# Performance work log

Hardware: AMD Instinct MI355X
Metric: run time of the kernel (lower is better)

The kernel has to match this reference:

```python
import jax, jax.numpy as jnp
import numpy as np

NUM_HEADS = 12
HEAD_DIM = 64
DROPKEY = 0.1
BN_EPS = 1e-5


def setup_inputs() -> dict:
    key = jax.random.key(0)
    ks = jax.random.split(key, 6)
    b, n, d = 4, 1024, 768
    img_c, hw = 256, 32
    x = jax.random.normal(ks[0], (b, n, d), dtype=jnp.float32)
    y = jax.random.normal(ks[1], (b, img_c, hw, hw), dtype=jnp.float32)
    drop_mask = jax.random.uniform(ks[2], (b, NUM_HEADS, n, n), dtype=jnp.float32)
    W_qkv = jax.random.normal(ks[3], (d, 3 * d), dtype=jnp.float32) * (d ** -0.5)
    conv1_w = jax.random.normal(ks[4], (img_c, 1, 3, 3), dtype=jnp.float32) * 0.1
    conv2_w = jax.random.normal(ks[5], (d, img_c, 1, 1), dtype=jnp.float32) * (img_c ** -0.5)
    bn_gamma = jnp.ones((d,), dtype=jnp.float32)
    bn_beta = jnp.zeros((d,), dtype=jnp.float32)
    return {"x": x, "y": y, "drop_mask": drop_mask, "W_qkv": W_qkv,
            "conv1_w": conv1_w, "conv2_w": conv2_w,
            "bn_gamma": bn_gamma, "bn_beta": bn_beta}


def reference(x, y, drop_mask, W_qkv, conv1_w, conv2_w, bn_gamma, bn_beta):
    b, n, d = x.shape
    h, hd = NUM_HEADS, HEAD_DIM
    scale = hd ** -0.5

    # --- attention branch ---
    qkv = x @ W_qkv                                     # [b, n, 3d]
    q, k, v = jnp.split(qkv, 3, axis=-1)
    def to_heads(t):
        return t.reshape(b, n, h, hd).transpose(0, 2, 1, 3)  # [b, h, n, hd]
    q, k, v = to_heads(q), to_heads(k), to_heads(v)
    scores = jnp.einsum('bhid,bhjd->bhij', q, k) * scale
    # dropkey: bernoulli(p) additive -1e12 mask before softmax
    mask = (drop_mask < DROPKEY).astype(scores.dtype)
    scores = scores + mask * jnp.asarray(-1e12, scores.dtype)
    attn = jax.nn.softmax(scores, axis=-1)
    out = jnp.einsum('bhij,bhjd->bhid', attn, v)        # [b, h, n, hd]
    out = out.transpose(0, 2, 1, 3).reshape(b, n, h * hd)

    # --- conv branch: depthwise 3x3 -> 1x1 -> BN(train) -> ReLU ---
    img_c = y.shape[1]
    y1 = jax.lax.conv_general_dilated(
        y, conv1_w, window_strides=(1, 1), padding='SAME',
        dimension_numbers=('NCHW', 'OIHW', 'NCHW'),
        feature_group_count=img_c)                      # [b, img_c, H, W]
    y2 = jax.lax.conv_general_dilated(
        y1, conv2_w, window_strides=(1, 1), padding='SAME',
        dimension_numbers=('NCHW', 'OIHW', 'NCHW'))     # [b, d, H, W]
    mean = jnp.mean(y2, axis=(0, 2, 3), keepdims=True)
    var = jnp.var(y2, axis=(0, 2, 3), keepdims=True)
    y_bn = (y2 - mean) * jax.lax.rsqrt(var + BN_EPS)
    y_bn = y_bn * bn_gamma[None, :, None, None] + bn_beta[None, :, None, None]
    y_out = jax.nn.relu(y_bn)                           # [b, d, H, W]

    # patchify(p1=p2=1) + flatten == 'b c h w -> b (h w) c'
    y_tok = y_out.transpose(0, 2, 3, 1).reshape(b, n, d)
    return (out + y_tok, y_out)


if __name__ == '__main__':
    inp = setup_inputs()
    o, yo = jax.jit(reference)(**inp)
    print(o.shape, yo.shape)
```

## Files before the change

kernel.cpp:

```cpp
#include <hip/hip_runtime.h>
#include <cstddef>

#define B_     4
#define NTOK   1024
#define DMODEL 768
#define NH     12
#define IMGC   256
#define NPIX   1024

typedef __attribute__((ext_vector_type(8))) short bf16x8;
typedef __attribute__((ext_vector_type(4))) float f32x4;
typedef __attribute__((ext_vector_type(8))) unsigned short u16x8;

static __device__ __forceinline__ unsigned short f2bf(float f) {
  unsigned int u = __float_as_uint(f);
  u += 0x7FFFu + ((u >> 16) & 1u);
  return (unsigned short)(u >> 16);
}

#define SWZ(row, b) (((row) << 7) + ((b) ^ (((row) & 7) << 4)))

#define GLOAD16(g, l) __builtin_amdgcn_global_load_lds(                      \
    (const __attribute__((address_space(1))) void*)(g),                      \
    (__attribute__((address_space(3))) void*)(l), 16, 0, 0)

__global__ __launch_bounds__(256) void k_cvt(const float* __restrict__ X,
                                             const float* __restrict__ Wqkv,
                                             const float* __restrict__ W2,
                                             unsigned short* __restrict__ Xb,
                                             unsigned short* __restrict__ Wtb,
                                             unsigned short* __restrict__ W2b,
                                             float* __restrict__ bnacc) {
  __shared__ unsigned short T[32][33];
  const int bid = blockIdx.x;
  const int t = threadIdx.x;
  if (bid < 1536) {
    const size_t i8 = (size_t)bid * 256 + t;
    const float4 a = *(const float4*)(X + i8 * 8);
    const float4 b = *(const float4*)(X + i8 * 8 + 4);
    u16x8 o;
    o[0] = f2bf(a.x); o[1] = f2bf(a.y); o[2] = f2bf(a.z); o[3] = f2bf(a.w);
    o[4] = f2bf(b.x); o[5] = f2bf(b.y); o[6] = f2bf(b.z); o[7] = f2bf(b.w);
    *(u16x8*)(Xb + i8 * 8) = o;
  } else if (bid < 3264) {
    const int b2 = bid - 1536;
    const int n0 = (b2 % 72) * 32, k0 = (b2 / 72) * 32;
    const int tx = t & 31, ty = t >> 5;
#pragma unroll
    for (int i = 0; i < 4; i++) {
      int kl = ty + i * 8;
      T[tx][kl] = f2bf(Wqkv[(size_t)(k0 + kl) * 2304 + n0 + tx]);
    }
    __syncthreads();
#pragma unroll
    for (int i = 0; i < 4; i++) {
      int nl = ty + i * 8;
      Wtb[(size_t)(n0 + nl) * 768 + k0 + tx] = T[nl][tx];
    }
  } else if (bid < 3360) {
    const size_t i8 = (size_t)(bid - 3264) * 256 + t;
    const float4 a = *(const float4*)(W2 + i8 * 8);
    const float4 b = *(const float4*)(W2 + i8 * 8 + 4);
    u16x8 o;
    o[0] = f2bf(a.x); o[1] = f2bf(a.y); o[2] = f2bf(a.z); o[3] = f2bf(a.w);
    o[4] = f2bf(b.x); o[5] = f2bf(b.y); o[6] = f2bf(b.z); o[7] = f2bf(b.w);
    *(u16x8*)(W2b + i8 * 8) = o;
  } else {
    for (int i = t; i < 1536; i += 256) bnacc[i] = 0.0f;
  }
}

__global__ __launch_bounds__(256) void k_qkv_gemm(const unsigned short* __restrict__ Xb,
                                                  const unsigned short* __restrict__ Wt,
                                                  unsigned short* __restrict__ q,
                                                  unsigned short* __restrict__ k,
                                                  unsigned short* __restrict__ v) {
  __shared__ __align__(16) char AsB[16384];
  __shared__ __align__(16) char BsB[16384];
  const int t = threadIdx.x;
  const int w = t >> 6, l = t & 63;
  const int r = l & 15, g = l >> 4;
  const int wr = w >> 1, wc = w & 1;
  const int m0 = blockIdx.y * 128;
  const int n0 = blockIdx.x * 128;
  const int rsel  = l >> 3;
  const int slotp = (l & 7) ^ (rsel & 7);
  f32x4 acc[4][4] = {};

  for (int step = 0; step < 12; ++step) {
    const int k0 = step * 64;
#pragma unroll
    for (int i = 0; i < 4; i++) {
      const int chunk = (i << 2) + w;
      const int row = (chunk << 3) + rsel;
      GLOAD16(Xb + (size_t)(m0 + row) * 768 + k0 + (slotp << 3),
              AsB + (chunk << 10) + (l << 4));
      GLOAD16(Wt + (size_t)(n0 + row) * 768 + k0 + (slotp << 3),
              BsB + (chunk << 10) + (l << 4));
    }
    __syncthreads();
#pragma unroll
    for (int kk = 0; kk < 2; kk++) {
      bf16x8 a[4], b[4];
#pragma unroll
      for (int m = 0; m < 4; m++) {
        const int row = wr * 64 + m * 16 + r;
        a[m] = *(const bf16x8*)(AsB + SWZ(row, kk * 64 + (g << 4)));
      }
#pragma unroll
      for (int n = 0; n < 4; n++) {
        const int row = wc * 64 + n * 16 + r;
        b[n] = *(const bf16x8*)(BsB + SWZ(row, kk * 64 + (g << 4)));
      }
#pragma unroll
      for (int m = 0; m < 4; m++)
#pragma unroll
        for (int n = 0; n < 4; n++)
          acc[m][n] = __builtin_amdgcn_mfma_f32_16x16x32_bf16(a[m], b[n], acc[m][n], 0, 0, 0);
    }
    __syncthreads();
  }

  const int which = blockIdx.x / 6;
  const int cbase = (blockIdx.x - which * 6) * 128 + wc * 64;
  unsigned short* dst = which == 0 ? q : (which == 1 ? k : v);
#pragma unroll
  for (int m = 0; m < 4; m++) {
    const int grow = m0 + wr * 64 + m * 16 + g * 4;
#pragma unroll
    for (int n = 0; n < 4; n++) {
      const int c = cbase + n * 16 + r;
      const int head = c >> 6, dim = c & 63;
#pragma unroll
      for (int reg = 0; reg < 4; reg++) {
        const int row = grow + reg;
        const int bb = row >> 10, tok = row & 1023;
        dst[((size_t)(((bb * NH + head) << 10) + tok) << 6) + dim] = f2bf(acc[m][n][reg]);
      }
    }
  }
}

__global__ __launch_bounds__(256) void k_attn(const unsigned short* __restrict__ qb,
                                              const unsigned short* __restrict__ kb,
                                              const unsigned short* __restrict__ vb,
                                              const float* __restrict__ dm,
                                              float* __restrict__ out0) {
  __shared__ __align__(16) unsigned short QsA[4096];
  __shared__ __align__(16) unsigned short KsA[4096];
  __shared__ __align__(16) unsigned short VtA[4096];
  __shared__ __align__(16) unsigned short PsA[4096];
  char* qs = (char*)QsA; char* ks = (char*)KsA;
  char* vt = (char*)VtA; char* ps = (char*)PsA;
  const int bh = blockIdx.x;
  const int qt = blockIdx.y;
  const int t  = threadIdx.x;
  const int w = t >> 6, l = t & 63, r = l & 15, g = l >> 4;
  const size_t hbase = (size_t)bh << 16;
  const char* qg = (const char*)(qb + hbase + ((size_t)qt << 12));
  const char* kg = (const char*)(kb + hbase);
  const char* vg = (const char*)(vb + hbase);
  const float* mp = dm + ((size_t)bh << 20) + ((size_t)(qt * 64) << 10);

#pragma unroll
  for (int i = 0; i < 2; i++) {
    int cid = t + (i << 8);
    int row = cid >> 3, slot = cid & 7;
    uint4 val = *(const uint4*)(qg + row * 128 + slot * 16);
    *(uint4*)(qs + SWZ(row, slot * 16)) = val;
  }

  float m_run[4] = {-INFINITY, -INFINITY, -INFINITY, -INFINITY};
  float l_run[4] = {0.0f, 0.0f, 0.0f, 0.0f};
  f32x4 O[4] = {};

  for (int kt = 0; kt < 16; kt++) {
    __syncthreads();
#pragma unroll
    for (int i = 0; i < 2; i++) {
      int cid = t + (i << 8);
      int row = cid >> 3, slot = cid & 7;
      uint4 val = *(const uint4*)(kg + (size_t)(kt * 64 + row) * 128 + slot * 16);
      *(uint4*)(ks + SWZ(row, slot * 16)) = val;
    }
    {
      int j = t & 63, dh = t >> 6;
      const char* vrow = vg + (size_t)(kt * 64 + j) * 128 + dh * 32;
      u16x8 v0 = *(const u16x8*)(vrow);
      u16x8 v1 = *(const u16x8*)(vrow + 16);
#pragma unroll
      for (int e = 0; e < 8; e++) {
        *(unsigned short*)(vt + SWZ(dh * 16 + e, 2 * j))     = v0[e];
        *(unsigned short*)(vt + SWZ(dh * 16 + 8 + e, 2 * j)) = v1[e];
      }
    }
    float md[4][4];
    {
      const float* mr = mp + (size_t)(w * 16 + g * 4) * 1024 + kt * 64 + r;
#pragma unroll
      for (int reg = 0; reg < 4; reg++)
#pragma unroll
        for (int jt = 0; jt < 4; jt++)
          md[reg][jt] = mr[reg * 1024 + jt * 16];
    }
    __syncthreads();

    f32x4 s[4] = {};
    bf16x8 aQ[2];
#pragma unroll
    for (int kc = 0; kc < 2; kc++)
      aQ[kc] = *(const bf16x8*)(qs + SWZ(w * 16 + r, kc * 64 + g * 16));
#pragma unroll
    for (int jt = 0; jt < 4; jt++) {
#pragma unroll
      for (int kc = 0; kc < 2; kc++) {
        bf16x8 bK = *(const bf16x8*)(ks + SWZ(jt * 16 + r, kc * 64 + g * 16));
        s[jt] = __builtin_amdgcn_mfma_f32_16x16x32_bf16(aQ[kc], bK, s[jt], 0, 0, 0);
      }
    }
    float sv[4][4];
#pragma unroll
    for (int jt = 0; jt < 4; jt++)
#pragma unroll
      for (int reg = 0; reg < 4; reg++)
        sv[jt][reg] = s[jt][reg] * 0.125f + (md[reg][jt] < 0.1f ? -1e12f : 0.0f);

    float alpha[4];
#pragma unroll
    for (int reg = 0; reg < 4; reg++) {
      float mt = fmaxf(fmaxf(sv[0][reg], sv[1][reg]), fmaxf(sv[2][reg], sv[3][reg]));
      mt = fmaxf(mt, __shfl_xor(mt, 1));
      mt = fmaxf(mt, __shfl_xor(mt, 2));
      mt = fmaxf(mt, __shfl_xor(mt, 4));
      mt = fmaxf(mt, __shfl_xor(mt, 8));
      float mn = fmaxf(m_run[reg], mt);
      alpha[reg] = __expf(m_run[reg] - mn);
      m_run[reg] = mn;
    }
#pragma unroll
    for (int reg = 0; reg < 4; reg++) {
      int row = w * 16 + g * 4 + reg;
      float ps_ = 0.0f;
#pragma unroll
      for (int jt = 0; jt < 4; jt++) {
        float p = __expf(sv[jt][reg] - m_run[reg]);
        ps_ += p;
        *(unsigned short*)(ps + SWZ(row, 2 * (jt * 16 + r))) = f2bf(p);
      }
      ps_ += __shfl_xor(ps_, 1);
      ps_ += __shfl_xor(ps_, 2);
      ps_ += __shfl_xor(ps_, 4);
      ps_ += __shfl_xor(ps_, 8);
      l_run[reg] = l_run[reg] * alpha[reg] + ps_;
    }
#pragma unroll
    for (int dt = 0; dt < 4; dt++)
#pragma unroll
      for (int reg = 0; reg < 4; reg++)
        O[dt][reg] *= alpha[reg];
    asm volatile("s_waitcnt lgkmcnt(0)" ::: "memory");
    __builtin_amdgcn_sched_barrier(0);
#pragma unroll
    for (int kc = 0; kc < 2; kc++) {
      bf16x8 aP = *(const bf16x8*)(ps + SWZ(w * 16 + r, kc * 64 + g * 16));
#pragma unroll
      for (int dt = 0; dt < 4; dt++) {
        bf16x8 bV = *(const bf16x8*)(vt + SWZ(dt * 16 + r, kc * 64 + g * 16));
        O[dt] = __builtin_amdgcn_mfma_f32_16x16x32_bf16(aP, bV, O[dt], 0, 0, 0);
      }
    }
  }
  const int bb = bh / NH, hh = bh % NH;
  float inv[4];
#pragma unroll
  for (int reg = 0; reg < 4; reg++) inv[reg] = 1.0f / l_run[reg];
  float* op = out0 + ((size_t)(bb * 1024 + qt * 64 + w * 16 + g * 4)) * 768 + hh * 64 + r;
#pragma unroll
  for (int reg = 0; reg < 4; reg++)
#pragma unroll
    for (int dt = 0; dt < 4; dt++)
      op[(size_t)reg * 768 + dt * 16] = O[dt][reg] * inv[reg];
}

__global__ __launch_bounds__(256) void k_dwconv(const float* __restrict__ y,
                                                const float* __restrict__ w1,
                                                float* __restrict__ y1) {
  const int bc = blockIdx.x;
  const int c = bc & 255;
  const float* yin = y + (size_t)bc * NPIX;
  float* yout = y1 + (size_t)bc * NPIX;
  float w[9];
#pragma unroll
  for (int i = 0; i < 9; i++) w[i] = w1[c * 9 + i];
  const int t = threadIdx.x;
#pragma unroll
  for (int rep = 0; rep < 4; rep++) {
    int px = t + rep * 256;
    int yy = px >> 5, xx = px & 31;
    float acc = 0.0f;
#pragma unroll
    for (int dy = -1; dy <= 1; dy++) {
      int sy = yy + dy;
      if (sy < 0 || sy > 31) continue;
#pragma unroll
      for (int dx = -1; dx <= 1; dx++) {
        int sx = xx + dx;
        if (sx < 0 || sx > 31) continue;
        acc = fmaf(yin[(sy << 5) + sx], w[(dy + 1) * 3 + dx + 1], acc);
      }
    }
    yout[px] = acc;
  }
}

__global__ __launch_bounds__(256) void k_trans(const float* __restrict__ y1,
                                               unsigned short* __restrict__ y1t) {
  __shared__ float T[64][65];
  const int p0 = blockIdx.x * 64, c0 = blockIdx.y * 64, b = blockIdx.z;
  const int t = threadIdx.x;
  const float* src = y1 + ((size_t)b << 18);
  {
    const int pl = t & 63, cl0 = t >> 6;
#pragma unroll
    for (int i = 0; i < 16; i++) {
      int cl = cl0 * 16 + i;
      T[cl][pl] = src[(size_t)(c0 + cl) * 1024 + p0 + pl];
    }
  }
  __syncthreads();
  {
    const int cl = t & 63, pl0 = t >> 6;
    unsigned short* dst = y1t + ((size_t)b << 18);
#pragma unroll
    for (int i = 0; i < 16; i++) {
      int pl = pl0 * 16 + i;
      dst[(size_t)(p0 + pl) * 256 + c0 + cl] = f2bf(T[cl][pl]);
    }
  }
}

__global__ __launch_bounds__(256) void k_c1x1(const unsigned short* __restrict__ W2b,
                                              const unsigned short* __restrict__ y1t,
                                              float* __restrict__ Y2,
                                              float* __restrict__ bn_sum,
                                              float* __restrict__ bn_sumsq) {
  __shared__ __align__(16) char AsB[16384];
  __shared__ __align__(16) char BsB[16384];
  const int t = threadIdx.x;
  const int w = t >> 6, l = t & 63;
  const int r = l & 15, g = l >> 4;
  const int wr = w >> 1, wc = w & 1;
  const int m0 = blockIdx.y * 128;
  const int n0 = blockIdx.x * 128;
  const int b  = blockIdx.z;
  const unsigned short* Bb = y1t + ((size_t)b << 18);
  const int rsel  = l >> 3;
  const int slotp = (l & 7) ^ (rsel & 7);
  f32x4 acc[4][4] = {};

  for (int step = 0; step < 4; ++step) {
    const int k0 = step * 64;
#pragma unroll
    for (int i = 0; i < 4; i++) {
      const int chunk = (i << 2) + w;
      const int row = (chunk << 3) + rsel;
      GLOAD16(W2b + (size_t)(m0 + row) * 256 + k0 + (slotp << 3),
              AsB + (chunk << 10) + (l << 4));
      GLOAD16(Bb + (size_t)(n0 + row) * 256 + k0 + (slotp << 3),
              BsB + (chunk << 10) + (l << 4));
    }
    __syncthreads();
#pragma unroll
    for (int kk = 0; kk < 2; kk++) {
      bf16x8 a[4], bfr[4];
#pragma unroll
      for (int m = 0; m < 4; m++) {
        const int row = wr * 64 + m * 16 + r;
        a[m] = *(const bf16x8*)(AsB + SWZ(row, kk * 64 + (g << 4)));
      }
#pragma unroll
      for (int n = 0; n < 4; n++) {
        const int row = wc * 64 + n * 16 + r;
        bfr[n] = *(const bf16x8*)(BsB + SWZ(row, kk * 64 + (g << 4)));
      }
#pragma unroll
      for (int m = 0; m < 4; m++)
#pragma unroll
        for (int n = 0; n < 4; n++)
          acc[m][n] = __builtin_amdgcn_mfma_f32_16x16x32_bf16(a[m], bfr[n], acc[m][n], 0, 0, 0);
    }
    __syncthreads();
  }

  float* Yb = Y2 + (((size_t)b * DMODEL) << 10);
#pragma unroll
  for (int m = 0; m < 4; m++) {
#pragma unroll
    for (int reg = 0; reg < 4; reg++) {
      const int oc = m0 + wr * 64 + m * 16 + g * 4 + reg;
      float s = 0.0f, sq = 0.0f;
#pragma unroll
      for (int n = 0; n < 4; n++) {
        const int p = n0 + wc * 64 + n * 16 + r;
        const float val = acc[m][n][reg];
        Yb[((size_t)oc << 10) + p] = val;
        s += val;
        sq = fmaf(val, val, sq);
      }
      s  += __shfl_xor(s, 1);  sq += __shfl_xor(sq, 1);
      s  += __shfl_xor(s, 2);  sq += __shfl_xor(sq, 2);
      s  += __shfl_xor(s, 4);  sq += __shfl_xor(sq, 4);
      s  += __shfl_xor(s, 8);  sq += __shfl_xor(sq, 8);
      if (r == 0) {
        atomicAdd(&bn_sum[oc], s);
        atomicAdd(&bn_sumsq[oc], sq);
      }
    }
  }
}

__global__ __launch_bounds__(256) void k_bnfuse(const float* __restrict__ y2,
                                                const float* __restrict__ bn_sum,
                                                const float* __restrict__ bn_sumsq,
                                                const float* __restrict__ gamma,
                                                const float* __restrict__ beta,
                                                float* __restrict__ out0,
                                                float* __restrict__ out1) {
  __shared__ float T[32][33];
  __shared__ float sc_l[32], sh_l[32];
  const int p0 = blockIdx.x * 32;
  const int c0 = blockIdx.y * 32;
  const int bb = blockIdx.z;
  const int tx = threadIdx.x;
  const int ty = threadIdx.y;
  const int tt = ty * 32 + tx;
  if (tt < 32) {
    const int c = c0 + tt;
    float S = bn_sum[c], SQ = bn_sumsq[c];
    float mean = S * (1.0f / 4096.0f);
    float var = SQ * (1.0f / 4096.0f) - mean * mean;
    float rstd = rsqrtf(var + 1e-5f);
    float s = gamma[c] * rstd;
    sc_l[tt] = s;
    sh_l[tt] = fmaf(-mean, s, beta[c]);
  }
  __syncthreads();
#pragma unroll
  for (int i = 0; i < 4; i++) {
    int cl = ty + 8 * i;
    int c = c0 + cl;
    size_t a = ((size_t)(bb * DMODEL + c) << 10) + p0 + tx;
    float val = fmaxf(fmaf(y2[a], sc_l[cl], sh_l[cl]), 0.0f);
    out1[a] = val;
    T[cl][tx] = val;
  }
  __syncthreads();
#pragma unroll
  for (int i = 0; i < 4; i++) {
    int pl = ty + 8 * i;
    size_t a = ((size_t)((bb << 10) + p0 + pl)) * DMODEL + c0 + tx;
    out0[a] += T[tx][pl];
  }
}

extern "C" void kernel_launch(void* const* d_in, const int* in_sizes, int n_in,
                              void* d_out, int out_size, void* d_ws, size_t ws_size,
                              hipStream_t stream) {
  (void)in_sizes; (void)n_in; (void)out_size; (void)ws_size;
  const float* x    = (const float*)d_in[0];
  const float* y    = (const float*)d_in[1];
  const float* dm   = (const float*)d_in[2];
  const float* wqkv = (const float*)d_in[3];
  const float* w1   = (const float*)d_in[4];
  const float* w2   = (const float*)d_in[5];
  const float* gam  = (const float*)d_in[6];
  const float* bet  = (const float*)d_in[7];
  float* out0 = (float*)d_out;
  float* out1 = out0 + (size_t)B_ * NTOK * DMODEL;

  char* wsb = (char*)d_ws;
  unsigned short* Xb  = (unsigned short*)wsb;
  unsigned short* Wtb = (unsigned short*)(wsb + 6291456);
  unsigned short* W2b = (unsigned short*)(wsb + 9830400);
  unsigned short* qb  = (unsigned short*)(wsb + 10223616);
  unsigned short* kb  = (unsigned short*)(wsb + 16515072);
  unsigned short* vb  = (unsigned short*)(wsb + 22806528);
  unsigned short* y1t = (unsigned short*)(wsb + 29097984);
  float* y2 = (float*)(wsb + 31195136);
  float* y1 = (float*)(wsb + 35389440);
  float* bnacc = (float*)(wsb + 43778048);
  float* bn_sum = bnacc;
  float* bn_sumsq = bnacc + 768;

  k_cvt<<<dim3(3361), 256, 0, stream>>>(x, wqkv, w2, Xb, Wtb, W2b, bnacc);
  k_dwconv<<<dim3(B_ * IMGC), 256, 0, stream>>>(y, w1, y1);
  k_trans<<<dim3(16, 4, B_), 256, 0, stream>>>(y1, y1t);
  k_c1x1<<<dim3(8, 6, B_), 256, 0, stream>>>(W2b, y1t, y2, bn_sum, bn_sumsq);
  k_qkv_gemm<<<dim3(18, 32), 256, 0, stream>>>(Xb, Wtb, qb, kb, vb);
  k_attn<<<dim3(48, 16), 256, 0, stream>>>(qb, kb, vb, dm, out0);
  k_bnfuse<<<dim3(32, 24, B_), dim3(32, 8), 0, stream>>>(y2, bn_sum, bn_sumsq, gam, bet, out0, out1);
}
```

Baseline: 128.9 us.

## Double-buffer LDS staging in GEMMs and attention, prefetch K/V and packed dropkey mask

Adds double-buffered shared-memory tiles to the QKV GEMM, the 1x1 conv GEMM and the attention kernel, so the next tile's global loads are issued while MFMAs run on the current tile. This removes one barrier per iteration. In attention, K moves to direct global-to-LDS loads and V/mask loads are prefetched into registers and written after the PV MFMAs. The float dropkey mask is compacted into per-row bit masks in LDS rather than each lane loading 16 scattered floats. The cost is doubled LDS use, which may lower occupancy, and higher register pressure from the prefetch values.

```diff
diff --git a/kernel.cpp b/kernel.cpp
--- a/kernel.cpp
+++ b/kernel.cpp
@@ -23,6 +23,19 @@
 #define GLOAD16(g, l) __builtin_amdgcn_global_load_lds(                      \
     (const __attribute__((address_space(1))) void*)(g),                      \
     (__attribute__((address_space(3))) void*)(l), 16, 0, 0)
+
+static __device__ __forceinline__ void stage_pair(const unsigned short* A0, int lda,
+                                                  const unsigned short* B0, int ldb,
+                                                  char* as, char* bs,
+                                                  int w, int l, int rsel, int slotp) {
+#pragma unroll
+  for (int i = 0; i < 4; i++) {
+    const int chunk = (i << 2) + w;
+    const int row = (chunk << 3) + rsel;
+    GLOAD16(A0 + (size_t)row * lda + (slotp << 3), as + (chunk << 10) + (l << 4));
+    GLOAD16(B0 + (size_t)row * ldb + (slotp << 3), bs + (chunk << 10) + (l << 4));
+  }
+}
 
 __global__ __launch_bounds__(256) void k_cvt(const float* __restrict__ X,
                                              const float* __restrict__ Wqkv,
@@ -75,8 +88,8 @@
                                                   unsigned short* __restrict__ q,
                                                   unsigned short* __restrict__ k,
                                                   unsigned short* __restrict__ v) {
-  __shared__ __align__(16) char AsB[16384];
-  __shared__ __align__(16) char BsB[16384];
+  __shared__ __align__(16) char AsB[2][16384];
+  __shared__ __align__(16) char BsB[2][16384];
   const int t = threadIdx.x;
   const int w = t >> 6, l = t & 63;
   const int r = l & 15, g = l >> 4;
@@ -85,32 +98,30 @@
   const int n0 = blockIdx.x * 128;
   const int rsel  = l >> 3;
   const int slotp = (l & 7) ^ (rsel & 7);
+  const unsigned short* A0 = Xb + (size_t)m0 * 768;
+  const unsigned short* B0 = Wt + (size_t)n0 * 768;
   f32x4 acc[4][4] = {};
 
+  stage_pair(A0, 768, B0, 768, AsB[0], BsB[0], w, l, rsel, slotp);
+  __syncthreads();
+
   for (int step = 0; step < 12; ++step) {
-    const int k0 = step * 64;
-#pragma unroll
-    for (int i = 0; i < 4; i++) {
-      const int chunk = (i << 2) + w;
-      const int row = (chunk << 3) + rsel;
-      GLOAD16(Xb + (size_t)(m0 + row) * 768 + k0 + (slotp << 3),
-              AsB + (chunk << 10) + (l << 4));
-      GLOAD16(Wt + (size_t)(n0 + row) * 768 + k0 + (slotp << 3),
-              BsB + (chunk << 10) + (l << 4));
-    }
-    __syncthreads();
+    const int cur = step & 1;
+    if (step < 11)
+      stage_pair(A0 + (step + 1) * 64, 768, B0 + (step + 1) * 64, 768,
+                 AsB[cur ^ 1], BsB[cur ^ 1], w, l, rsel, slotp);
 #pragma unroll
     for (int kk = 0; kk < 2; kk++) {
       bf16x8 a[4], b[4];
 #pragma unroll
       for (int m = 0; m < 4; m++) {
         const int row = wr * 64 + m * 16 + r;
-        a[m] = *(const bf16x8*)(AsB + SWZ(row, kk * 64 + (g << 4)));
+        a[m] = *(const bf16x8*)(AsB[cur] + SWZ(row, kk * 64 + (g << 4)));
       }
 #pragma unroll
       for (int n = 0; n < 4; n++) {
         const int row = wc * 64 + n * 16 + r;
-        b[n] = *(const bf16x8*)(BsB + SWZ(row, kk * 64 + (g << 4)));
+        b[n] = *(const bf16x8*)(BsB[cur] + SWZ(row, kk * 64 + (g << 4)));
       }
 #pragma unroll
       for (int m = 0; m < 4; m++)
@@ -147,11 +158,12 @@
                                               const float* __restrict__ dm,
                                               float* __restrict__ out0) {
   __shared__ __align__(16) unsigned short QsA[4096];
-  __shared__ __align__(16) unsigned short KsA[4096];
-  __shared__ __align__(16) unsigned short VtA[4096];
+  __shared__ __align__(16) unsigned short KsA[2][4096];
+  __shared__ __align__(16) unsigned short VtA[2][4096];
   __shared__ __align__(16) unsigned short PsA[4096];
-  char* qs = (char*)QsA; char* ks = (char*)KsA;
-  char* vt = (char*)VtA; char* ps = (char*)PsA;
+  __shared__ __align__(8) unsigned short MbA[2][64][4];
+  char* qs = (char*)QsA;
+  char* ps = (char*)PsA;
   const int bh = blockIdx.x;
   const int qt = blockIdx.y;
   const int t  = threadIdx.x;
@@ -162,6 +174,11 @@
   const char* vg = (const char*)(vb + hbase);
   const float* mp = dm + ((size_t)bh << 20) + ((size_t)(qt * 64) << 10);
 
+  const int mrow = t >> 2, mq = t & 3;
+  const float* mrow_p = mp + (size_t)mrow * 1024 + mq * 16;
+  const int rsel = l >> 3;
+  const int kslotp = (l & 7) ^ (rsel & 7);
+
 #pragma unroll
   for (int i = 0; i < 2; i++) {
     int cid = t + (i << 8);
@@ -169,52 +186,83 @@
     uint4 val = *(const uint4*)(qg + row * 128 + slot * 16);
     *(uint4*)(qs + SWZ(row, slot * 16)) = val;
   }
+#pragma unroll
+  for (int i = 0; i < 2; i++) {
+    const int chunk = (i << 2) + w;
+    const int row = (chunk << 3) + rsel;
+    GLOAD16(kg + (size_t)row * 128 + kslotp * 16,
+            (char*)KsA[0] + (chunk << 10) + (l << 4));
+  }
+  {
+    u16x8 v0 = *(const u16x8*)(vg + (size_t)l * 128 + w * 32);
+    u16x8 v1 = *(const u16x8*)(vg + (size_t)l * 128 + w * 32 + 16);
+    float4 nm0 = *(const float4*)(mrow_p);
+    float4 nm1 = *(const float4*)(mrow_p + 4);
+    float4 nm2 = *(const float4*)(mrow_p + 8);
+    float4 nm3 = *(const float4*)(mrow_p + 12);
+    char* vt0 = (char*)VtA[0];
+#pragma unroll
+    for (int e = 0; e < 8; e++) {
+      *(unsigned short*)(vt0 + SWZ(w * 16 + e, 2 * l))     = v0[e];
+      *(unsigned short*)(vt0 + SWZ(w * 16 + 8 + e, 2 * l)) = v1[e];
+    }
+    unsigned bits = 0;
+    bits |= (nm0.x < 0.1f) << 0;  bits |= (nm0.y < 0.1f) << 1;
+    bits |= (nm0.z < 0.1f) << 2;  bits |= (nm0.w < 0.1f) << 3;
+    bits |= (nm1.x < 0.1f) << 4;  bits |= (nm1.y < 0.1f) << 5;
+    bits |= (nm1.z < 0.1f) << 6;  bits |= (nm1.w < 0.1f) << 7;
+    bits |= (nm2.x < 0.1f) << 8;  bits |= (nm2.y < 0.1f) << 9;
+    bits |= (nm2.z < 0.1f) << 10; bits |= (nm2.w < 0.1f) << 11;
+    bits |= (nm3.x < 0.1f) << 12; bits |= (nm3.y < 0.1f) << 13;
+    bits |= (nm3.z < 0.1f) << 14; bits |= (nm3.w < 0.1f) << 15;
+    MbA[0][mrow][mq] = (unsigned short)bits;
+  }
+  __syncthreads();
+
+  bf16x8 aQ[2];
+#pragma unroll
+  for (int kc = 0; kc < 2; kc++)
+    aQ[kc] = *(const bf16x8*)(qs + SWZ(w * 16 + r, kc * 64 + g * 16));
 
   float m_run[4] = {-INFINITY, -INFINITY, -INFINITY, -INFINITY};
   float l_run[4] = {0.0f, 0.0f, 0.0f, 0.0f};
   f32x4 O[4] = {};
 
   for (int kt = 0; kt < 16; kt++) {
-    __syncthreads();
-#pragma unroll
-    for (int i = 0; i < 2; i++) {
-      int cid = t + (i << 8);
-      int row = cid >> 3, slot = cid & 7;
-      uint4 val = *(const uint4*)(kg + (size_t)(kt * 64 + row) * 128 + slot * 16);
-      *(uint4*)(ks + SWZ(row, slot * 16)) = val;
-    }
-    {
-      int j = t & 63, dh = t >> 6;
-      const char* vrow = vg + (size_t)(kt * 64 + j) * 128 + dh * 32;
-      u16x8 v0 = *(const u16x8*)(vrow);
-      u16x8 v1 = *(const u16x8*)(vrow + 16);
-#pragma unroll
-      for (int e = 0; e < 8; e++) {
-        *(unsigned short*)(vt + SWZ(dh * 16 + e, 2 * j))     = v0[e];
-        *(unsigned short*)(vt + SWZ(dh * 16 + 8 + e, 2 * j)) = v1[e];
-      }
-    }
-    float md[4][4];
-    {
-      const float* mr = mp + (size_t)(w * 16 + g * 4) * 1024 + kt * 64 + r;
-#pragma unroll
-      for (int reg = 0; reg < 4; reg++)
-#pragma unroll
-        for (int jt = 0; jt < 4; jt++)
-          md[reg][jt] = mr[reg * 1024 + jt * 16];
-    }
-    __syncthreads();
+    const int cur = kt & 1, nxt = cur ^ 1;
+    u16x8 nv0, nv1;
+    float4 nm0, nm1, nm2, nm3;
+    if (kt < 15) {
+      const size_t roff = (size_t)((kt + 1) * 64);
+#pragma unroll
+      for (int i = 0; i < 2; i++) {
+        const int chunk = (i << 2) + w;
+        const int row = (chunk << 3) + rsel;
+        GLOAD16(kg + (roff + row) * 128 + kslotp * 16,
+                (char*)KsA[nxt] + (chunk << 10) + (l << 4));
+      }
+      nv0 = *(const u16x8*)(vg + (roff + l) * 128 + w * 32);
+      nv1 = *(const u16x8*)(vg + (roff + l) * 128 + w * 32 + 16);
+      const float* mrp = mrow_p + (kt + 1) * 64;
+      nm0 = *(const float4*)(mrp);
+      nm1 = *(const float4*)(mrp + 4);
+      nm2 = *(const float4*)(mrp + 8);
+      nm3 = *(const float4*)(mrp + 12);
+    }
+    unsigned short mbq[4][4];
+#pragma unroll
+    for (int reg = 0; reg < 4; reg++) {
+      ushort4 m4 = *(const ushort4*)&MbA[cur][w * 16 + g * 4 + reg][0];
+      mbq[reg][0] = m4.x; mbq[reg][1] = m4.y; mbq[reg][2] = m4.z; mbq[reg][3] = m4.w;
+    }
 
     f32x4 s[4] = {};
-    bf16x8 aQ[2];
-#pragma unroll
-    for (int kc = 0; kc < 2; kc++)
-      aQ[kc] = *(const bf16x8*)(qs + SWZ(w * 16 + r, kc * 64 + g * 16));
+    char* ksc = (char*)KsA[cur];
 #pragma unroll
     for (int jt = 0; jt < 4; jt++) {
 #pragma unroll
       for (int kc = 0; kc < 2; kc++) {
-        bf16x8 bK = *(const bf16x8*)(ks + SWZ(jt * 16 + r, kc * 64 + g * 16));
+        bf16x8 bK = *(const bf16x8*)(ksc + SWZ(jt * 16 + r, kc * 64 + g * 16));
         s[jt] = __builtin_amdgcn_mfma_f32_16x16x32_bf16(aQ[kc], bK, s[jt], 0, 0, 0);
       }
     }
@@ -222,8 +270,10 @@
 #pragma unroll
     for (int jt = 0; jt < 4; jt++)
 #pragma unroll
-      for (int reg = 0; reg < 4; reg++)
-        sv[jt][reg] = s[jt][reg] * 0.125f + (md[reg][jt] < 0.1f ? -1e12f : 0.0f);
+      for (int reg = 0; reg < 4; reg++) {
+        const float pen = ((mbq[reg][jt] >> r) & 1) ? -1e12f : 0.0f;
+        sv[jt][reg] = fmaf(s[jt][reg], 0.125f, pen);
+      }
 
     float alpha[4];
 #pragma unroll
@@ -260,16 +310,37 @@
         O[dt][reg] *= alpha[reg];
     asm volatile("s_waitcnt lgkmcnt(0)" ::: "memory");
     __builtin_amdgcn_sched_barrier(0);
+    char* vtc = (char*)VtA[cur];
 #pragma unroll
     for (int kc = 0; kc < 2; kc++) {
       bf16x8 aP = *(const bf16x8*)(ps + SWZ(w * 16 + r, kc * 64 + g * 16));
 #pragma unroll
       for (int dt = 0; dt < 4; dt++) {
-        bf16x8 bV = *(const bf16x8*)(vt + SWZ(dt * 16 + r, kc * 64 + g * 16));
+        bf16x8 bV = *(const bf16x8*)(vtc + SWZ(dt * 16 + r, kc * 64 + g * 16));
         O[dt] = __builtin_amdgcn_mfma_f32_16x16x32_bf16(aP, bV, O[dt], 0, 0, 0);
       }
     }
-  }
+    if (kt < 15) {
+      char* vtn = (char*)VtA[nxt];
+#pragma unroll
+      for (int e = 0; e < 8; e++) {
+        *(unsigned short*)(vtn + SWZ(w * 16 + e, 2 * l))     = nv0[e];
+        *(unsigned short*)(vtn + SWZ(w * 16 + 8 + e, 2 * l)) = nv1[e];
+      }
+      unsigned bits = 0;
+      bits |= (nm0.x < 0.1f) << 0;  bits |= (nm0.y < 0.1f) << 1;
+      bits |= (nm0.z < 0.1f) << 2;  bits |= (nm0.w < 0.1f) << 3;
+      bits |= (nm1.x < 0.1f) << 4;  bits |= (nm1.y < 0.1f) << 5;
+      bits |= (nm1.z < 0.1f) << 6;  bits |= (nm1.w < 0.1f) << 7;
+      bits |= (nm2.x < 0.1f) << 8;  bits |= (nm2.y < 0.1f) << 9;
+      bits |= (nm2.z < 0.1f) << 10; bits |= (nm2.w < 0.1f) << 11;
+      bits |= (nm3.x < 0.1f) << 12; bits |= (nm3.y < 0.1f) << 13;
+      bits |= (nm3.z < 0.1f) << 14; bits |= (nm3.w < 0.1f) << 15;
+      MbA[nxt][mrow][mq] = (unsigned short)bits;
+    }
+    __syncthreads();
+  }
+
   const int bb = bh / NH, hh = bh % NH;
   float inv[4];
 #pragma unroll
@@ -344,8 +415,8 @@
                                               float* __restrict__ Y2,
                                               float* __restrict__ bn_sum,
                                               float* __restrict__ bn_sumsq) {
-  __shared__ __align__(16) char AsB[16384];
-  __shared__ __align__(16) char BsB[16384];
+  __shared__ __align__(16) char AsB[2][16384];
+  __shared__ __align__(16) char BsB[2][16384];
   const int t = threadIdx.x;
   const int w = t >> 6, l = t & 63;
   const int r = l & 15, g = l >> 4;
@@ -353,35 +424,32 @@
   const int m0 = blockIdx.y * 128;
   const int n0 = blockIdx.x * 128;
   const int b  = blockIdx.z;
-  const unsigned short* Bb = y1t + ((size_t)b << 18);
+  const unsigned short* A0 = W2b + (size_t)m0 * 256;
+  const unsigned short* B0 = y1t + ((size_t)b << 18) + (size_t)n0 * 256;
   const int rsel  = l >> 3;
   const int slotp = (l & 7) ^ (rsel & 7);
   f32x4 acc[4][4] = {};
 
+  stage_pair(A0, 256, B0, 256, AsB[0], BsB[0], w, l, rsel, slotp);
+  __syncthreads();
+
   for (int step = 0; step < 4; ++step) {
-    const int k0 = step * 64;
-#pragma unroll
-    for (int i = 0; i < 4; i++) {
-      const int chunk = (i << 2) + w;
-      const int row = (chunk << 3) + rsel;
-      GLOAD16(W2b + (size_t)(m0 + row) * 256 + k0 + (slotp << 3),
-              AsB + (chunk << 10) + (l << 4));
-      GLOAD16(Bb + (size_t)(n0 + row) * 256 + k0 + (slotp << 3),
-              BsB + (chunk << 10) + (l << 4));
-    }
-    __syncthreads();
+    const int cur = step & 1;
+    if (step < 3)
+      stage_pair(A0 + (step + 1) * 64, 256, B0 + (step + 1) * 64, 256,
+                 AsB[cur ^ 1], BsB[cur ^ 1], w, l, rsel, slotp);
 #pragma unroll
     for (int kk = 0; kk < 2; kk++) {
       bf16x8 a[4], bfr[4];
 #pragma unroll
       for (int m = 0; m < 4; m++) {
         const int row = wr * 64 + m * 16 + r;
-        a[m] = *(const bf16x8*)(AsB + SWZ(row, kk * 64 + (g << 4)));
+        a[m] = *(const bf16x8*)(AsB[cur] + SWZ(row, kk * 64 + (g << 4)));
       }
 #pragma unroll
       for (int n = 0; n < 4; n++) {
         const int row = wc * 64 + n * 16 + r;
-        bfr[n] = *(const bf16x8*)(BsB + SWZ(row, kk * 64 + (g << 4)));
+        bfr[n] = *(const bf16x8*)(BsB[cur] + SWZ(row, kk * 64 + (g << 4)));
       }
 #pragma unroll
       for (int m = 0; m < 4; m++)
```

New measurement: 141.7 us. +9.9%, slower.

## Double-buffer K tiles via async global-to-LDS loads and prefetch V in registers

Applied to the files above, without the earlier changes.

The attention kernel now keeps Q in registers, loaded once, which frees its LDS buffer to serve as a second K buffer. The next K tile is fetched with asynchronous global_load_lds into the alternate buffer, and the next V tile is prefetched into registers during the current tile's compute. Both are meant to hide global memory latency behind the MFMA and softmax work. This adds an extra barrier per iteration for the V transpose store and raises register pressure.

```diff
diff --git a/kernel.cpp b/kernel.cpp
--- a/kernel.cpp
+++ b/kernel.cpp
@@ -146,12 +146,12 @@
                                               const unsigned short* __restrict__ vb,
                                               const float* __restrict__ dm,
                                               float* __restrict__ out0) {
-  __shared__ __align__(16) unsigned short QsA[4096];
-  __shared__ __align__(16) unsigned short KsA[4096];
+  __shared__ __align__(16) unsigned short K0A[4096];
+  __shared__ __align__(16) unsigned short K1A[4096];
   __shared__ __align__(16) unsigned short VtA[4096];
   __shared__ __align__(16) unsigned short PsA[4096];
-  char* qs = (char*)QsA; char* ks = (char*)KsA;
-  char* vt = (char*)VtA; char* ps = (char*)PsA;
+  char* ps = (char*)PsA;
+  char* vt = (char*)VtA;
   const int bh = blockIdx.x;
   const int qt = blockIdx.y;
   const int t  = threadIdx.x;
@@ -162,59 +162,83 @@
   const char* vg = (const char*)(vb + hbase);
   const float* mp = dm + ((size_t)bh << 20) + ((size_t)(qt * 64) << 10);
 
+  const int rsel = l >> 3;
+  const int kslotp = (l & 7) ^ (rsel & 7);
+  const float* mr_base = mp + (size_t)(w * 16 + g * 4) * 1024 + r;
+
+  {
+    char* qs = (char*)K1A;
+#pragma unroll
+    for (int i = 0; i < 2; i++) {
+      int cid = t + (i << 8);
+      int row = cid >> 3, slot = cid & 7;
+      uint4 val = *(const uint4*)(qg + row * 128 + slot * 16);
+      *(uint4*)(qs + SWZ(row, slot * 16)) = val;
+    }
+  }
 #pragma unroll
   for (int i = 0; i < 2; i++) {
-    int cid = t + (i << 8);
-    int row = cid >> 3, slot = cid & 7;
-    uint4 val = *(const uint4*)(qg + row * 128 + slot * 16);
-    *(uint4*)(qs + SWZ(row, slot * 16)) = val;
-  }
+    const int chunk = (i << 2) + w;
+    const int row = (chunk << 3) + rsel;
+    GLOAD16(kg + (size_t)row * 128 + kslotp * 16,
+            (char*)K0A + (chunk << 10) + (l << 4));
+  }
+  {
+    u16x8 v0 = *(const u16x8*)(vg + (size_t)l * 128 + w * 32);
+    u16x8 v1 = *(const u16x8*)(vg + (size_t)l * 128 + w * 32 + 16);
+#pragma unroll
+    for (int e = 0; e < 8; e++) {
+      *(unsigned short*)(vt + SWZ(w * 16 + e, 2 * l))     = v0[e];
+      *(unsigned short*)(vt + SWZ(w * 16 + 8 + e, 2 * l)) = v1[e];
+    }
+  }
+  __syncthreads();
+
+  bf16x8 aQ[2];
+#pragma unroll
+  for (int kc = 0; kc < 2; kc++)
+    aQ[kc] = *(const bf16x8*)((char*)K1A + SWZ(w * 16 + r, kc * 64 + g * 16));
+  asm volatile("s_waitcnt lgkmcnt(0)" ::: "memory");
+  __builtin_amdgcn_sched_barrier(0);
+  __syncthreads();
 
   float m_run[4] = {-INFINITY, -INFINITY, -INFINITY, -INFINITY};
   float l_run[4] = {0.0f, 0.0f, 0.0f, 0.0f};
   f32x4 O[4] = {};
 
   for (int kt = 0; kt < 16; kt++) {
-    __syncthreads();
-#pragma unroll
-    for (int i = 0; i < 2; i++) {
-      int cid = t + (i << 8);
-      int row = cid >> 3, slot = cid & 7;
-      uint4 val = *(const uint4*)(kg + (size_t)(kt * 64 + row) * 128 + slot * 16);
-      *(uint4*)(ks + SWZ(row, slot * 16)) = val;
-    }
-    {
-      int j = t & 63, dh = t >> 6;
-      const char* vrow = vg + (size_t)(kt * 64 + j) * 128 + dh * 32;
-      u16x8 v0 = *(const u16x8*)(vrow);
-      u16x8 v1 = *(const u16x8*)(vrow + 16);
-#pragma unroll
-      for (int e = 0; e < 8; e++) {
-        *(unsigned short*)(vt + SWZ(dh * 16 + e, 2 * j))     = v0[e];
-        *(unsigned short*)(vt + SWZ(dh * 16 + 8 + e, 2 * j)) = v1[e];
-      }
+    const int cur = kt & 1;
+    char* ksc = cur ? (char*)K1A : (char*)K0A;
+    char* ksn = cur ? (char*)K0A : (char*)K1A;
+    u16x8 nv0, nv1;
+    if (kt < 15) {
+      const size_t roff = (size_t)((kt + 1) * 64);
+#pragma unroll
+      for (int i = 0; i < 2; i++) {
+        const int chunk = (i << 2) + w;
+        const int row = (chunk << 3) + rsel;
+        GLOAD16(kg + (roff + row) * 128 + kslotp * 16,
+                ksn + (chunk << 10) + (l << 4));
+      }
+      nv0 = *(const u16x8*)(vg + (roff + l) * 128 + w * 32);
+      nv1 = *(const u16x8*)(vg + (roff + l) * 128 + w * 32 + 16);
     }
     float md[4][4];
     {
-      const float* mr = mp + (size_t)(w * 16 + g * 4) * 1024 + kt * 64 + r;
+      const float* mr = mr_base + kt * 64;
 #pragma unroll
       for (int reg = 0; reg < 4; reg++)
 #pragma unroll
         for (int jt = 0; jt < 4; jt++)
           md[reg][jt] = mr[reg * 1024 + jt * 16];
     }
-    __syncthreads();
 
     f32x4 s[4] = {};
-    bf16x8 aQ[2];
-#pragma unroll
-    for (int kc = 0; kc < 2; kc++)
-      aQ[kc] = *(const bf16x8*)(qs + SWZ(w * 16 + r, kc * 64 + g * 16));
 #pragma unroll
     for (int jt = 0; jt < 4; jt++) {
 #pragma unroll
       for (int kc = 0; kc < 2; kc++) {
-        bf16x8 bK = *(const bf16x8*)(ks + SWZ(jt * 16 + r, kc * 64 + g * 16));
+        bf16x8 bK = *(const bf16x8*)(ksc + SWZ(jt * 16 + r, kc * 64 + g * 16));
         s[jt] = __builtin_amdgcn_mfma_f32_16x16x32_bf16(aQ[kc], bK, s[jt], 0, 0, 0);
       }
     }
@@ -269,7 +293,17 @@
         O[dt] = __builtin_amdgcn_mfma_f32_16x16x32_bf16(aP, bV, O[dt], 0, 0, 0);
       }
     }
-  }
+    __syncthreads();
+    if (kt < 15) {
+#pragma unroll
+      for (int e = 0; e < 8; e++) {
+        *(unsigned short*)(vt + SWZ(w * 16 + e, 2 * l))     = nv0[e];
+        *(unsigned short*)(vt + SWZ(w * 16 + 8 + e, 2 * l)) = nv1[e];
+      }
+      __syncthreads();
+    }
+  }
+
   const int bb = bh / NH, hh = bh % NH;
   float inv[4];
 #pragma unroll
```

Result: slower. 133.7 us (+3.7%).

## Fuse BN-ReLU residual add into attention epilogue and dwconv into convert kernel

Applied to the files above, without the earlier changes.

The depthwise conv now runs as extra blocks of the conversion kernel, which removes one launch. The attention epilogue reads y2 directly, applies the BN scale/shift and ReLU, and adds the result into out0 as it is written. This avoids a separate read-modify-write pass over out0 with a transpose. A simpler vectorized kernel now writes only out1. The trade-off is that the attention epilogue does extra strided loads of y2, and y2 is read twice overall.

```diff
diff --git a/kernel.cpp b/kernel.cpp
--- a/kernel.cpp
+++ b/kernel.cpp
@@ -27,9 +27,12 @@
 __global__ __launch_bounds__(256) void k_cvt(const float* __restrict__ X,
                                              const float* __restrict__ Wqkv,
                                              const float* __restrict__ W2,
+                                             const float* __restrict__ Yimg,
+                                             const float* __restrict__ w1,
                                              unsigned short* __restrict__ Xb,
                                              unsigned short* __restrict__ Wtb,
                                              unsigned short* __restrict__ W2b,
+                                             float* __restrict__ y1,
                                              float* __restrict__ bnacc) {
   __shared__ unsigned short T[32][33];
   const int bid = blockIdx.x;
@@ -65,8 +68,34 @@
     o[0] = f2bf(a.x); o[1] = f2bf(a.y); o[2] = f2bf(a.z); o[3] = f2bf(a.w);
     o[4] = f2bf(b.x); o[5] = f2bf(b.y); o[6] = f2bf(b.z); o[7] = f2bf(b.w);
     *(u16x8*)(W2b + i8 * 8) = o;
+  } else if (bid == 3360) {
+    for (int i = t; i < 1536; i += 256) bnacc[i] = 0.0f;
   } else {
-    for (int i = t; i < 1536; i += 256) bnacc[i] = 0.0f;
+    const int bc = bid - 3361;
+    const int c = bc & 255;
+    const float* yin = Yimg + (size_t)bc * NPIX;
+    float* yout = y1 + (size_t)bc * NPIX;
+    float w[9];
+#pragma unroll
+    for (int i = 0; i < 9; i++) w[i] = w1[c * 9 + i];
+#pragma unroll
+    for (int rep = 0; rep < 4; rep++) {
+      int px = t + rep * 256;
+      int yy = px >> 5, xx = px & 31;
+      float acc = 0.0f;
+#pragma unroll
+      for (int dy = -1; dy <= 1; dy++) {
+        int sy = yy + dy;
+        if (sy < 0 || sy > 31) continue;
+#pragma unroll
+        for (int dx = -1; dx <= 1; dx++) {
+          int sx = xx + dx;
+          if (sx < 0 || sx > 31) continue;
+          acc = fmaf(yin[(sy << 5) + sx], w[(dy + 1) * 3 + dx + 1], acc);
+        }
+      }
+      yout[px] = acc;
+    }
   }
 }
 
@@ -145,6 +174,11 @@
                                               const unsigned short* __restrict__ kb,
                                               const unsigned short* __restrict__ vb,
                                               const float* __restrict__ dm,
+                                              const float* __restrict__ y2,
+                                              const float* __restrict__ bn_sum,
+                                              const float* __restrict__ bn_sumsq,
+                                              const float* __restrict__ gamma,
+                                              const float* __restrict__ beta,
                                               float* __restrict__ out0) {
   __shared__ __align__(16) unsigned short QsA[4096];
   __shared__ __align__(16) unsigned short KsA[4096];
@@ -274,43 +308,33 @@
   float inv[4];
 #pragma unroll
   for (int reg = 0; reg < 4; reg++) inv[reg] = 1.0f / l_run[reg];
-  float* op = out0 + ((size_t)(bb * 1024 + qt * 64 + w * 16 + g * 4)) * 768 + hh * 64 + r;
+  float scv[4], shv[4];
+#pragma unroll
+  for (int dt = 0; dt < 4; dt++) {
+    const int c = hh * 64 + dt * 16 + r;
+    const float S = bn_sum[c], SQ = bn_sumsq[c];
+    const float mean = S * (1.0f / 4096.0f);
+    const float var = SQ * (1.0f / 4096.0f) - mean * mean;
+    const float rstd = rsqrtf(var + 1e-5f);
+    const float sc = gamma[c] * rstd;
+    scv[dt] = sc;
+    shv[dt] = fmaf(-mean, sc, beta[c]);
+  }
+  const int prow = qt * 64 + w * 16 + g * 4;
+  const float* y2p = y2 + (((size_t)(bb * DMODEL + hh * 64 + r)) << 10) + prow;
+  float4 yq[4];
+#pragma unroll
+  for (int dt = 0; dt < 4; dt++)
+    yq[dt] = *(const float4*)(y2p + ((size_t)dt << 14));
+  float* op = out0 + ((size_t)(bb * 1024 + prow)) * 768 + hh * 64 + r;
 #pragma unroll
   for (int reg = 0; reg < 4; reg++)
 #pragma unroll
-    for (int dt = 0; dt < 4; dt++)
-      op[(size_t)reg * 768 + dt * 16] = O[dt][reg] * inv[reg];
-}
-
-__global__ __launch_bounds__(256) void k_dwconv(const float* __restrict__ y,
-                                                const float* __restrict__ w1,
-                                                float* __restrict__ y1) {
-  const int bc = blockIdx.x;
-  const int c = bc & 255;
-  const float* yin = y + (size_t)bc * NPIX;
-  float* yout = y1 + (size_t)bc * NPIX;
-  float w[9];
-#pragma unroll
-  for (int i = 0; i < 9; i++) w[i] = w1[c * 9 + i];
-  const int t = threadIdx.x;
-#pragma unroll
-  for (int rep = 0; rep < 4; rep++) {
-    int px = t + rep * 256;
-    int yy = px >> 5, xx = px & 31;
-    float acc = 0.0f;
-#pragma unroll
-    for (int dy = -1; dy <= 1; dy++) {
-      int sy = yy + dy;
-      if (sy < 0 || sy > 31) continue;
-#pragma unroll
-      for (int dx = -1; dx <= 1; dx++) {
-        int sx = xx + dx;
-        if (sx < 0 || sx > 31) continue;
-        acc = fmaf(yin[(sy << 5) + sx], w[(dy + 1) * 3 + dx + 1], acc);
-      }
-    }
-    yout[px] = acc;
-  }
+    for (int dt = 0; dt < 4; dt++) {
+      const float yv = (&yq[dt].x)[reg];
+      const float ytok = fmaxf(fmaf(yv, scv[dt], shv[dt]), 0.0f);
+      op[(size_t)reg * 768 + dt * 16] = fmaf(O[dt][reg], inv[reg], ytok);
+    }
 }
 
 __global__ __launch_bounds__(256) void k_trans(const float* __restrict__ y1,
@@ -419,48 +443,29 @@
   }
 }
 
-__global__ __launch_bounds__(256) void k_bnfuse(const float* __restrict__ y2,
+__global__ __launch_bounds__(256) void k_bnout1(const float* __restrict__ y2,
                                                 const float* __restrict__ bn_sum,
                                                 const float* __restrict__ bn_sumsq,
                                                 const float* __restrict__ gamma,
                                                 const float* __restrict__ beta,
-                                                float* __restrict__ out0,
                                                 float* __restrict__ out1) {
-  __shared__ float T[32][33];
-  __shared__ float sc_l[32], sh_l[32];
-  const int p0 = blockIdx.x * 32;
-  const int c0 = blockIdx.y * 32;
-  const int bb = blockIdx.z;
-  const int tx = threadIdx.x;
-  const int ty = threadIdx.y;
-  const int tt = ty * 32 + tx;
-  if (tt < 32) {
-    const int c = c0 + tt;
-    float S = bn_sum[c], SQ = bn_sumsq[c];
-    float mean = S * (1.0f / 4096.0f);
-    float var = SQ * (1.0f / 4096.0f) - mean * mean;
-    float rstd = rsqrtf(var + 1e-5f);
-    float s = gamma[c] * rstd;
-    sc_l[tt] = s;
-    sh_l[tt] = fmaf(-mean, s, beta[c]);
-  }
-  __syncthreads();
-#pragma unroll
-  for (int i = 0; i < 4; i++) {
-    int cl = ty + 8 * i;
-    int c = c0 + cl;
-    size_t a = ((size_t)(bb * DMODEL + c) << 10) + p0 + tx;
-    float val = fmaxf(fmaf(y2[a], sc_l[cl], sh_l[cl]), 0.0f);
-    out1[a] = val;
-    T[cl][tx] = val;
-  }
-  __syncthreads();
-#pragma unroll
-  for (int i = 0; i < 4; i++) {
-    int pl = ty + 8 * i;
-    size_t a = ((size_t)((bb << 10) + p0 + pl)) * DMODEL + c0 + tx;
-    out0[a] += T[tx][pl];
-  }
+  const int row = blockIdx.x;
+  const int c = row % DMODEL;
+  const int t = threadIdx.x;
+  const float S = bn_sum[c], SQ = bn_sumsq[c];
+  const float mean = S * (1.0f / 4096.0f);
+  const float var = SQ * (1.0f / 4096.0f) - mean * mean;
+  const float rstd = rsqrtf(var + 1e-5f);
+  const float sc = gamma[c] * rstd;
+  const float sh = fmaf(-mean, sc, beta[c]);
+  const float* src = y2 + ((size_t)row << 10) + t * 4;
+  float* dst = out1 + ((size_t)row << 10) + t * 4;
+  float4 v = *(const float4*)src;
+  v.x = fmaxf(fmaf(v.x, sc, sh), 0.0f);
+  v.y = fmaxf(fmaf(v.y, sc, sh), 0.0f);
+  v.z = fmaxf(fmaf(v.z, sc, sh), 0.0f);
+  v.w = fmaxf(fmaf(v.w, sc, sh), 0.0f);
+  *(float4*)dst = v;
 }
 
 extern "C" void kernel_launch(void* const* d_in, const int* in_sizes, int n_in,
@@ -492,11 +497,10 @@
   float* bn_sum = bnacc;
   float* bn_sumsq = bnacc + 768;
 
-  k_cvt<<<dim3(3361), 256, 0, stream>>>(x, wqkv, w2, Xb, Wtb, W2b, bnacc);
-  k_dwconv<<<dim3(B_ * IMGC), 256, 0, stream>>>(y, w1, y1);
+  k_cvt<<<dim3(4385), 256, 0, stream>>>(x, wqkv, w2, y, w1, Xb, Wtb, W2b, y1, bnacc);
   k_trans<<<dim3(16, 4, B_), 256, 0, stream>>>(y1, y1t);
   k_c1x1<<<dim3(8, 6, B_), 256, 0, stream>>>(W2b, y1t, y2, bn_sum, bn_sumsq);
   k_qkv_gemm<<<dim3(18, 32), 256, 0, stream>>>(Xb, Wtb, qb, kb, vb);
-  k_attn<<<dim3(48, 16), 256, 0, stream>>>(qb, kb, vb, dm, out0);
-  k_bnfuse<<<dim3(32, 24, B_), dim3(32, 8), 0, stream>>>(y2, bn_sum, bn_sumsq, gam, bet, out0, out1);
-}
+  k_attn<<<dim3(48, 16), 256, 0, stream>>>(qb, kb, vb, dm, y2, bn_sum, bn_sumsq, gam, bet, out0);
+  k_bnout1<<<dim3(B_ * DMODEL), 256, 0, stream>>>(y2, bn_sum, bn_sumsq, gam, bet, out1);
+}
```

Result: no change. 128.0 us (-0.7%).
